# Kernel optimization log

Measured on AMD Instinct MI355X. Metric: run time of the kernel, lower is better.

Reference implementation:

```python
import jax, jax.numpy as jnp
import numpy as np

TEMP_LEN = 16
TARGET_LEN = 22
DIM = 768
HEADS = 12
B = 16
NT = TEMP_LEN * TEMP_LEN          # 256 template tokens
NG = TARGET_LEN * TARGET_LEN      # 484 target tokens
N = NT + NG                       # 740
POS_HID = 512


def _gaussian_heatmap(center, size, sig=1.0):
    x_axis = np.linspace(0, size[0] - 1, size[0]) - center[0]
    y_axis = np.linspace(0, size[1] - 1, size[1]) - center[1]
    xx, yy = np.meshgrid(x_axis, y_axis)
    return np.exp(-0.5 * (xx ** 2 + yy ** 2) / sig ** 2)


def _bias_index(L):
    # faithful to getBiasIndex (w_len == h_len here)
    coords = np.stack(np.meshgrid(np.arange(L), np.arange(L), indexing='ij'))  # [2,L,L]
    flat = coords.reshape(2, -1)                                               # [2,L*L]
    rel = (flat[:, :, None] - flat[:, None, :]).transpose(1, 2, 0).astype(np.int64)
    rel[:, :, 0] += L - 1
    rel[:, :, 1] += L - 1
    rel[:, :, 0] *= 2 * L - 1
    return rel.sum(-1)  # [L*L, L*L]


def setup_inputs() -> dict:
    key = jax.random.key(0)
    ks = jax.random.split(key, 12)
    f32 = jnp.float32
    x = jax.random.normal(ks[0], (B, N, DIM), dtype=f32)
    temp_q = jax.random.normal(ks[1], (B, NT, DIM), dtype=f32)
    target_q = jax.random.normal(ks[2], (B, NG, DIM), dtype=f32)
    # linear weights stored [in, out] (transposed torch layout)
    w = lambda k, i, o: jax.random.normal(k, (i, o), dtype=f32) * 0.02
    q_w = w(ks[3], DIM, DIM)
    k_w = w(ks[4], DIM, DIM)
    v_w = w(ks[5], DIM, DIM)
    proj_w = w(ks[6], DIM, DIM)
    proj_b = jnp.zeros((DIM,), dtype=f32)
    rpb_table = jax.random.normal(ks[7], ((2 * TARGET_LEN - 1) ** 2, HEADS), dtype=f32) * 0.0002
    rpb_table_temp = jax.random.normal(ks[8], ((2 * TEMP_LEN - 1) ** 2, HEADS), dtype=f32) * 0.0002
    pos_w1 = w(ks[9], 2, POS_HID)
    pos_b1 = jnp.zeros((POS_HID,), dtype=f32)
    pos_w2 = w(ks[10], POS_HID, HEADS)
    pos_b2 = jnp.zeros((HEADS,), dtype=f32)
    # deterministic cross-bias coordinate table (non-learned buffer)
    temp_tab = _gaussian_heatmap((TEMP_LEN // 2, TEMP_LEN // 2), (TEMP_LEN, TEMP_LEN)).astype(np.float32).flatten() \
        + np.linspace(-0.2, 0.2, NT, dtype=np.float32)
    targ_tab = _gaussian_heatmap((TARGET_LEN // 2, TARGET_LEN // 2), (TARGET_LEN, TARGET_LEN)).astype(np.float32).flatten() \
        + np.linspace(-0.2, 0.2, NG, dtype=np.float32)
    # torch.meshgrid default indexing='ij': [2, NT, NG] -> permute(1,2,0) -> [NT,NG,2]
    temp_target = np.stack(np.meshgrid(temp_tab, targ_tab, indexing='ij')).transpose(1, 2, 0)
    target_temp_tab = jnp.asarray(temp_target.transpose(1, 0, 2))  # [NG, NT, 2]
    temp_idx = jnp.asarray(_bias_index(TEMP_LEN))       # [NT, NT] int64
    target_idx = jnp.asarray(_bias_index(TARGET_LEN))   # [NG, NG] int64
    return {
        'x': x, 'temp_q': temp_q, 'target_q': target_q,
        'q_w': q_w, 'k_w': k_w, 'v_w': v_w, 'proj_w': proj_w, 'proj_b': proj_b,
        'rpb_table': rpb_table, 'rpb_table_temp': rpb_table_temp,
        'pos_w1': pos_w1, 'pos_b1': pos_b1, 'pos_w2': pos_w2, 'pos_b2': pos_b2,
        'target_temp_tab': target_temp_tab,
        'temp_idx': temp_idx, 'target_idx': target_idx,
    }


def reference(x, temp_q, target_q, q_w, k_w, v_w, proj_w, proj_b,
              rpb_table, rpb_table_temp, pos_w1, pos_b1, pos_w2, pos_b2,
              target_temp_tab, temp_idx, target_idx):
    Bsz, Ntok, C = x.shape
    H = HEADS
    hd = C // H
    scale = hd ** -0.5

    q_in = jnp.concatenate([temp_q, target_q], axis=1)                 # [B,N,C]
    q = (q_in @ q_w).reshape(Bsz, Ntok, H, hd).transpose(0, 2, 1, 3)   # [B,H,N,hd]
    k = (x @ k_w).reshape(Bsz, Ntok, H, hd).transpose(0, 2, 1, 3)
    v = (x @ v_w).reshape(Bsz, Ntok, H, hd).transpose(0, 2, 1, 3)

    # gathered relative position biases -> [H, Ni, Ni]
    temp_rpb = rpb_table_temp[temp_idx.reshape(-1)].reshape(NT, NT, H).transpose(2, 0, 1)
    targ_rpb = rpb_table[target_idx.reshape(-1)].reshape(NG, NG, H).transpose(2, 0, 1)
    # MLP cross bias: [NG, NT, 2] -> [NG, NT, H] -> [H, NG, NT]
    hid = jax.nn.relu(target_temp_tab @ pos_w1 + pos_b1)
    target_temp_bias = (hid @ pos_w2 + pos_b2).transpose(2, 0, 1)      # [H,NG,NT]
    temp_target_bias = target_temp_bias.transpose(0, 2, 1)             # [H,NT,NG]
    top = jnp.concatenate([temp_rpb, temp_target_bias], axis=2)        # [H,NT,N]
    bot = jnp.concatenate([target_temp_bias, targ_rpb], axis=2)        # [H,NG,N]
    bias = jnp.concatenate([top, bot], axis=1)[None]                   # [1,H,N,N]

    attn = jnp.einsum('bhnd,bhmd->bhnm', q, k) * scale + bias
    attn = jax.nn.softmax(attn, axis=-1)
    out = jnp.einsum('bhnm,bhmd->bhnd', attn, v).transpose(0, 2, 1, 3).reshape(Bsz, Ntok, C)
    return out @ proj_w + proj_b
```

## Files before the change

kernel.cpp:

```cpp
#include <hip/hip_runtime.h>


typedef unsigned short u16;
typedef short bf16x8 __attribute__((ext_vector_type(8)));
typedef float f32x4 __attribute__((ext_vector_type(4)));

#define BSZ   16
#define NTOK  740
#define NTMP  256
#define NTGT  484
#define DIMC  768
#define NHEAD 12
#define HDIM  64
#define MROWS (BSZ*NTOK)
#define SMAX  16.0f

__device__ __forceinline__ float bf2f(u16 u) {
    return __uint_as_float(((unsigned int)u) << 16);
}
__device__ __forceinline__ float bflo(unsigned int u) {
    return __uint_as_float(u << 16);
}
__device__ __forceinline__ float bfhi(unsigned int u) {
    return __uint_as_float(u & 0xffff0000u);
}
__device__ __forceinline__ u16 f2bf(float f) {
    unsigned int u = __float_as_uint(f);
    u += 0x7fffu + ((u >> 16) & 1u);
    return (u16)(u >> 16);
}

__device__ __forceinline__ void gl_lds16(const u16* g, u16* l) {
    __builtin_amdgcn_global_load_lds(
        (const __attribute__((address_space(1))) unsigned int*)(unsigned long long)g,
        (__attribute__((address_space(3))) unsigned int*)(unsigned int)(unsigned long long)l,
        16, 0, 0);
}

__device__ __forceinline__ size_t b2off(int h, int i, int j) {
    return ((size_t)(h * NTOK + i)) * 768 + ((j >> 6) << 6) + ((j & 15) << 2) + ((j >> 4) & 3);
}

#define PREP_CONV 4440
#define PREP_TRW  (PREP_CONV + 576)
#define PREP_DIAG (PREP_TRW + 2220)
#define PREP_ALL  (PREP_DIAG + 484)

__global__ __launch_bounds__(256) void prep_kernel(
    const float* __restrict__ x, const float* __restrict__ tq,
    const float* __restrict__ gq, u16* __restrict__ XB, u16* __restrict__ QB,
    const float* __restrict__ w0, const float* __restrict__ w1,
    const float* __restrict__ w2, const float* __restrict__ w3,
    u16* __restrict__ Wt,
    const float* __restrict__ rpb, const float* __restrict__ rpbt,
    const int* __restrict__ tidx, const int* __restrict__ gidx,
    const float* __restrict__ pw1, const float* __restrict__ pb1,
    const float* __restrict__ pw2, const float* __restrict__ pb2,
    const float* __restrict__ tab, u16* __restrict__ bias)
{
    __shared__ float T[64][65];
    const int blk = blockIdx.x;
    const int tid = threadIdx.x;

    if (blk < PREP_CONV) {
        int c = blk * 256 + tid;
        {
            const float* s = x + (size_t)c * 8;
            float4 p0 = *(const float4*)s, p1 = *(const float4*)(s + 4);
            u16 e[8] = {f2bf(p0.x), f2bf(p0.y), f2bf(p0.z), f2bf(p0.w),
                        f2bf(p1.x), f2bf(p1.y), f2bf(p1.z), f2bf(p1.w)};
            *(uint4*)(XB + (size_t)c * 8) = *(uint4*)e;
        }
        {
            int row = c / 96, cc = (c - row * 96) * 8;
            int b = row / NTOK, n = row - b * NTOK;
            const float* s = (n < NTMP)
                           ? tq + ((size_t)(b * NTMP + n)) * DIMC + cc
                           : gq + ((size_t)(b * NTGT + (n - NTMP))) * DIMC + cc;
            float4 p0 = *(const float4*)s, p1 = *(const float4*)(s + 4);
            u16 e[8] = {f2bf(p0.x), f2bf(p0.y), f2bf(p0.z), f2bf(p0.w),
                        f2bf(p1.x), f2bf(p1.y), f2bf(p1.z), f2bf(p1.w)};
            *(uint4*)(QB + (size_t)row * DIMC + cc) = *(uint4*)e;
        }
    } else if (blk < PREP_TRW) {
        int t = blk - PREP_CONV;
        int z = t / 144, rem = t - z * 144;
        int bx = rem % 12, by = rem / 12;
        const float* src = (z == 0) ? w0 : (z == 1) ? w1 : (z == 2) ? w2 : w3;
        const float scale = (z == 0) ? 0.125f : 1.0f;
        u16* dst = Wt + (size_t)z * DIMC * DIMC;
        int out0 = bx * 64, in0 = by * 64;
        #pragma unroll
        for (int l = 0; l < 4; l++) {
            int u = tid + (l << 8);
            int r = u >> 4, c4 = (u & 15) << 2;
            float4 p = *(const float4*)(src + (size_t)(in0 + r) * DIMC + out0 + c4);
            T[r][c4] = p.x; T[r][c4 + 1] = p.y; T[r][c4 + 2] = p.z; T[r][c4 + 3] = p.w;
        }
        __syncthreads();
        #pragma unroll
        for (int l = 0; l < 2; l++) {
            int u = tid + (l << 8);
            int r = u >> 3, c8 = (u & 7) << 3;
            u16 e[8];
            #pragma unroll
            for (int i = 0; i < 8; i++) e[i] = f2bf(T[c8 + i][r] * scale);
            *(uint4*)(dst + (size_t)(out0 + r) * DIMC + in0 + c8) = *(uint4*)e;
        }
    } else if (blk < PREP_DIAG) {
        int t = blk - PREP_TRW;
        int jb = t % 3, i = t / 3;
        int j = jb * 256 + tid;
        u16 vals[NHEAD];
        if (j >= NTOK) {
            u16 neg = f2bf(-1e30f);
            #pragma unroll
            for (int h = 0; h < NHEAD; h++) vals[h] = neg;
        } else if (i < NTMP && j < NTMP) {
            int idx = tidx[i * NTMP + j];
            #pragma unroll
            for (int h = 0; h < NHEAD; h++) vals[h] = f2bf(rpbt[idx * NHEAD + h]);
        } else if (i >= NTMP && j >= NTMP) {
            int idx = gidx[(i - NTMP) * NTGT + (j - NTMP)];
            #pragma unroll
            for (int h = 0; h < NHEAD; h++) vals[h] = f2bf(rpb[idx * NHEAD + h]);
        } else {
            return;
        }
        #pragma unroll
        for (int h = 0; h < NHEAD; h++) bias[b2off(h, i, j)] = vals[h];
    } else {
        int g = blk - PREP_DIAG;
        int t = tid;
        float a  = tab[(g * NTMP + t) * 2 + 0];
        float bb = tab[(g * NTMP + t) * 2 + 1];
        float acc[NHEAD];
        #pragma unroll
        for (int h = 0; h < NHEAD; h++) acc[h] = pb2[h];
        for (int k = 0; k < 512; k++) {
            float hid = fmaxf(a * pw1[k] + bb * pw1[512 + k] + pb1[k], 0.0f);
            #pragma unroll
            for (int h = 0; h < NHEAD; h++) acc[h] += hid * pw2[k * NHEAD + h];
        }
        #pragma unroll
        for (int h = 0; h < NHEAD; h++) {
            u16 v = f2bf(acc[h]);
            bias[b2off(h, t, NTMP + g)] = v;
            bias[b2off(h, NTMP + g, t)] = v;
        }
    }
}

template<int MODE>
__global__ __launch_bounds__(256) void gemm_bf16(
    const u16* __restrict__ A, const u16* __restrict__ Wt,
    const float* __restrict__ pb, u16* __restrict__ C0,
    u16* __restrict__ C1, float* __restrict__ Cf)
{
    __shared__ __align__(16) u16 As[8192];
    __shared__ __align__(16) u16 Bs[8192];
    const int tid = threadIdx.x;
    const int lane = tid & 63, w = tid >> 6;
    const int quad = lane >> 4, ln = lane & 15;
    const int m0 = blockIdx.y << 7;
    const int wm = (w >> 1) << 6, wn = (w & 1) << 6;

    const int nn = blockIdx.x << 7;
    const u16* Wbase = Wt + (size_t)nn * DIMC;
    u16* Cb;
    int col0;
    if (MODE == 1) {
        if (nn < DIMC) { col0 = nn; Cb = C0; }
        else           { col0 = nn - DIMC; Cb = C1; }
    } else {
        col0 = nn; Cb = C0;
    }

    f32x4 acc[4][4];
    #pragma unroll
    for (int i = 0; i < 4; i++)
        #pragma unroll
        for (int j = 0; j < 4; j++)
            acc[i][j] = (f32x4){0.f, 0.f, 0.f, 0.f};

    for (int k0 = 0; k0 < DIMC; k0 += 64) {
        __syncthreads();
        #pragma unroll
        for (int l = 0; l < 4; l++) {
            int f = tid + (l << 8);
            int c8 = f >> 7, r = f & 127;
            int grow = m0 + r; if (grow >= MROWS) grow = MROWS - 1;
            gl_lds16(A + (size_t)grow * DIMC + k0 + c8 * 8, As + f * 8);
            gl_lds16(Wbase + (size_t)r * DIMC + k0 + c8 * 8, Bs + f * 8);
        }
        __syncthreads();
        #pragma unroll
        for (int kp = 0; kp < 2; kp++) {
            bf16x8 af[4], bfr[4];
            #pragma unroll
            for (int mt = 0; mt < 4; mt++)
                af[mt] = *(const bf16x8*)&As[(((kp << 2) + quad) * 128 + wm + mt * 16 + ln) * 8];
            #pragma unroll
            for (int nt = 0; nt < 4; nt++)
                bfr[nt] = *(const bf16x8*)&Bs[(((kp << 2) + quad) * 128 + wn + nt * 16 + ln) * 8];
            #pragma unroll
            for (int mt = 0; mt < 4; mt++)
                #pragma unroll
                for (int nt = 0; nt < 4; nt++)
                    acc[mt][nt] = __builtin_amdgcn_mfma_f32_16x16x32_bf16(
                        af[mt], bfr[nt], acc[mt][nt], 0, 0, 0);
        }
    }

    #pragma unroll
    for (int mt = 0; mt < 4; mt++) {
        #pragma unroll
        for (int reg = 0; reg < 4; reg++) {
            int grow = m0 + wm + mt * 16 + (quad << 2) + reg;
            if (grow >= MROWS) continue;
            #pragma unroll
            for (int nt = 0; nt < 4; nt++) {
                int gcol = col0 + wn + nt * 16 + ln;
                float v = acc[mt][nt][reg];
                if (MODE == 2) {
                    Cf[(size_t)grow * DIMC + gcol] = v + pb[gcol];
                } else {
                    Cb[(size_t)grow * DIMC + gcol] = f2bf(v);
                }
            }
        }
    }
}

__global__ __launch_bounds__(256) void attn_mfma(
    const u16* __restrict__ Qg, const u16* __restrict__ Kg,
    const u16* __restrict__ Vg, const u16* __restrict__ bias,
    u16* __restrict__ ctx)
{
    __shared__ __align__(16) u16 KsL[4096];
    __shared__ __align__(16) u16 VtL[64 * 72];
    __shared__ __align__(16) u16 Pw[8][16][72];

    const int tid = threadIdx.x;
    const int lane = tid & 63, w = tid >> 6;
    const int quad = lane >> 4, ln = lane & 15;
    const int b = blockIdx.z, h = blockIdx.y;
    const int q0 = blockIdx.x << 7;
    const int mbase = q0 + (w << 5);
    const u16* bp = bias + ((size_t)h * NTOK) * 768;

    bf16x8 aq[2][2];
    #pragma unroll
    for (int mi = 0; mi < 2; mi++) {
        int qrow = mbase + (mi << 4) + ln; if (qrow >= NTOK) qrow = NTOK - 1;
        #pragma unroll
        for (int kp = 0; kp < 2; kp++)
            aq[mi][kp] = *(const bf16x8*)(Qg + ((size_t)(b * NTOK + qrow)) * DIMC
                                          + h * HDIM + kp * 32 + (quad << 3));
    }
    int boff[2][4];
    #pragma unroll
    for (int mi = 0; mi < 2; mi++)
        #pragma unroll
        for (int reg = 0; reg < 4; reg++) {
            int rr = mbase + (mi << 4) + (quad << 2) + reg;
            if (rr >= NTOK) rr = NTOK - 1;
            boff[mi][reg] = rr * 768 + (ln << 2);
        }

    const int pswz = ((ln >> 2) & 3) << 4;

    float rs[2][4] = {};
    f32x4 O[2][4];
    #pragma unroll
    for (int mi = 0; mi < 2; mi++)
        #pragma unroll
        for (int dt = 0; dt < 4; dt++) O[mi][dt] = (f32x4){0.f, 0.f, 0.f, 0.f};

    for (int j0 = 0; j0 < NTOK; j0 += 64) {
        __syncthreads();
        #pragma unroll
        for (int l = 0; l < 2; l++) {
            int f = tid + (l << 8);
            int chunk = f >> 6, jr = f & 63;
            int krow = j0 + jr; if (krow >= NTOK) krow = NTOK - 1;
            gl_lds16(Kg + ((size_t)(b * NTOK + krow)) * DIMC + h * HDIM + chunk * 8,
                     KsL + f * 8);
        }
        uint2 bvv[2][4];
        #pragma unroll
        for (int mi = 0; mi < 2; mi++)
            #pragma unroll
            for (int reg = 0; reg < 4; reg++)
                bvv[mi][reg] = *(const uint2*)(bp + boff[mi][reg] + j0);
        #pragma unroll
        for (int l = 0; l < 2; l++) {
            int u = tid + (l << 8);
            int jr = u >> 3, d0 = (u & 7) << 3;
            int vrow = j0 + jr; if (vrow >= NTOK) vrow = NTOK - 1;
            uint4 p = *(const uint4*)(Vg + ((size_t)(b * NTOK + vrow)) * DIMC + h * HDIM + d0);
            const u16* pe = (const u16*)&p;
            int jswz = jr ^ d0;
            #pragma unroll
            for (int i = 0; i < 8; i++) VtL[(d0 + i) * 72 + jswz] = pe[i];
        }
        __syncthreads();

        bf16x8 bv[4][2];
        #pragma unroll
        for (int dt = 0; dt < 4; dt++) {
            int key8 = ((dt * 2 + (ln >> 3)) & 7) << 3;
            #pragma unroll
            for (int kp = 0; kp < 2; kp++) {
                int koff = (kp * 32 + (quad << 3)) ^ key8;
                bv[dt][kp] = *(const bf16x8*)&VtL[(dt * 16 + ln) * 72 + koff];
            }
        }

        f32x4 s[2][4];
        #pragma unroll
        for (int mi = 0; mi < 2; mi++)
            #pragma unroll
            for (int nt = 0; nt < 4; nt++) s[mi][nt] = (f32x4){0.f, 0.f, 0.f, 0.f};
        #pragma unroll
        for (int kp = 0; kp < 2; kp++)
            #pragma unroll
            for (int nt = 0; nt < 4; nt++) {
                bf16x8 bk = *(const bf16x8*)
                    &KsL[(((kp << 2) + quad) * 64 + nt * 16 + ln) * 8];
                s[0][nt] = __builtin_amdgcn_mfma_f32_16x16x32_bf16(aq[0][kp], bk, s[0][nt], 0, 0, 0);
                s[1][nt] = __builtin_amdgcn_mfma_f32_16x16x32_bf16(aq[1][kp], bk, s[1][nt], 0, 0, 0);
            }

        #pragma unroll
        for (int mi = 0; mi < 2; mi++) {
            #pragma unroll
            for (int reg = 0; reg < 4; reg++) {
                uint2 bb = bvv[mi][reg];
                float p0 = __expf(s[mi][0][reg] + bflo(bb.x) - SMAX);
                float p1 = __expf(s[mi][1][reg] + bfhi(bb.x) - SMAX);
                float p2 = __expf(s[mi][2][reg] + bflo(bb.y) - SMAX);
                float p3 = __expf(s[mi][3][reg] + bfhi(bb.y) - SMAX);
                s[mi][0][reg] = p0; s[mi][1][reg] = p1;
                s[mi][2][reg] = p2; s[mi][3][reg] = p3;
                rs[mi][reg] += p0 + p1 + p2 + p3;
            }
            u16* pwb = &Pw[(w << 1) + mi][0][0];
            #pragma unroll
            for (int nt = 0; nt < 4; nt++) {
                int colw = ((nt ^ quad) << 4) + ln;
                #pragma unroll
                for (int reg = 0; reg < 4; reg++)
                    pwb[((quad << 2) + reg) * 72 + colw] = f2bf(s[mi][nt][reg]);
            }
            bf16x8 ap[2];
            #pragma unroll
            for (int kp = 0; kp < 2; kp++) {
                int koff = (kp * 32 + (quad << 3)) ^ pswz;
                ap[kp] = *(const bf16x8*)&pwb[ln * 72 + koff];
            }
            #pragma unroll
            for (int dt = 0; dt < 4; dt++)
                #pragma unroll
                for (int kp = 0; kp < 2; kp++)
                    O[mi][dt] = __builtin_amdgcn_mfma_f32_16x16x32_bf16(
                        ap[kp], bv[dt][kp], O[mi][dt], 0, 0, 0);
        }
    }

    #pragma unroll
    for (int mi = 0; mi < 2; mi++) {
        #pragma unroll
        for (int reg = 0; reg < 4; reg++) {
            float t = rs[mi][reg];
            #pragma unroll
            for (int mk = 8; mk >= 1; mk >>= 1) t += __shfl_xor(t, mk);
            float inv = 1.0f / t;
            int row = mbase + (mi << 4) + (quad << 2) + reg;
            if (row < NTOK) {
                #pragma unroll
                for (int dt = 0; dt < 4; dt++)
                    ctx[((size_t)(b * NTOK + row)) * DIMC + h * HDIM + dt * 16 + ln]
                        = f2bf(O[mi][dt][reg] * inv);
            }
        }
    }
}

extern "C" void kernel_launch(void* const* d_in, const int* in_sizes, int n_in,
                              void* d_out, int out_size, void* d_ws, size_t ws_size,
                              hipStream_t stream)
{
    const float* x        = (const float*)d_in[0];
    const float* temp_q   = (const float*)d_in[1];
    const float* target_q = (const float*)d_in[2];
    const float* q_w      = (const float*)d_in[3];
    const float* k_w      = (const float*)d_in[4];
    const float* v_w      = (const float*)d_in[5];
    const float* proj_w   = (const float*)d_in[6];
    const float* proj_b   = (const float*)d_in[7];
    const float* rpb      = (const float*)d_in[8];
    const float* rpbt     = (const float*)d_in[9];
    const float* pw1      = (const float*)d_in[10];
    const float* pb1      = (const float*)d_in[11];
    const float* pw2      = (const float*)d_in[12];
    const float* pb2      = (const float*)d_in[13];
    const float* tab      = (const float*)d_in[14];
    const int*   tidx     = (const int*)d_in[15];
    const int*   gidx     = (const int*)d_in[16];
    float* out = (float*)d_out;

    char* ws = (char*)d_ws;
    const size_t S = (size_t)MROWS * DIMC * sizeof(u16);
    const size_t SZB = (size_t)NHEAD * NTOK * 768 * sizeof(u16);
    u16* XB    = (u16*)(ws);
    u16* QB    = (u16*)(ws + S);
    u16* Q     = (u16*)(ws + 2 * S);
    u16* K     = (u16*)(ws + 3 * S);
    u16* V     = QB;
    u16* CTX   = XB;
    u16* BIAS2 = (u16*)(ws + 4 * S);
    u16* WT    = (u16*)(ws + 4 * S + SZB);

    prep_kernel<<<dim3(PREP_ALL), 256, 0, stream>>>(
        x, temp_q, target_q, XB, QB,
        q_w, k_w, v_w, proj_w, WT,
        rpb, rpbt, tidx, gidx,
        pw1, pb1, pw2, pb2, tab, BIAS2);

    const u16* WTq = WT;
    const u16* WTk = WT + (size_t)DIMC * DIMC;
    const u16* WTp = WT + 3 * (size_t)DIMC * DIMC;

    gemm_bf16<0><<<dim3(6, 93), 256, 0, stream>>>(QB, WTq, nullptr, Q, nullptr, nullptr);
    gemm_bf16<1><<<dim3(12, 93), 256, 0, stream>>>(XB, WTk, nullptr, K, V, nullptr);
    attn_mfma<<<dim3(6, 12, 16), 256, 0, stream>>>(Q, K, V, BIAS2, CTX);
    gemm_bf16<2><<<dim3(6, 93), 256, 0, stream>>>(CTX, WTp, proj_b, nullptr, nullptr, out);
}
```

Before: 496.4 us.

## Double-buffer GEMM LDS tiles and remap workgroups across XCDs

The GEMM main loop now uses two LDS buffers so the next K-tile's global-to-LDS loads are issued while the current tile is being multiplied. This hides load latency and removes one barrier per iteration. Workgroup IDs are also remapped so that consecutive tiles land on the same XCD, which should improve L2 reuse of the shared A/W tiles. The cost is doubled LDS use (64KB per block), which may lower occupancy. Whether the async loads truly overlap depends on how waitcnt is handled around the barriers.

Result: faster. 469.4 us (-5.4%).

```diff
diff --git a/kernel.cpp b/kernel.cpp
--- a/kernel.cpp
+++ b/kernel.cpp
@@ -157,15 +157,25 @@
     const float* __restrict__ pb, u16* __restrict__ C0,
     u16* __restrict__ C1, float* __restrict__ Cf)
 {
-    __shared__ __align__(16) u16 As[8192];
-    __shared__ __align__(16) u16 Bs[8192];
+    __shared__ __align__(16) u16 As[2][8192];
+    __shared__ __align__(16) u16 Bs[2][8192];
     const int tid = threadIdx.x;
     const int lane = tid & 63, w = tid >> 6;
     const int quad = lane >> 4, ln = lane & 15;
-    const int m0 = blockIdx.y << 7;
+
+    const int gx = gridDim.x;
+    const int nwg = gx * (int)gridDim.y;
+    const int flat = blockIdx.y * gx + blockIdx.x;
+    const int q = nwg >> 3, r = nwg & 7;
+    const int xcd = flat & 7, sidx = flat >> 3;
+    const int wg = (xcd < r) ? xcd * (q + 1) + sidx
+                             : r * (q + 1) + (xcd - r) * q + sidx;
+    const int by = wg / gx, bx = wg - by * gx;
+
+    const int m0 = by << 7;
     const int wm = (w >> 1) << 6, wn = (w & 1) << 6;
 
-    const int nn = blockIdx.x << 7;
+    const int nn = bx << 7;
     const u16* Wbase = Wt + (size_t)nn * DIMC;
     u16* Cb;
     int col0;
@@ -183,34 +193,50 @@
         for (int j = 0; j < 4; j++)
             acc[i][j] = (f32x4){0.f, 0.f, 0.f, 0.f};
 
-    for (int k0 = 0; k0 < DIMC; k0 += 64) {
+#define STAGE(s, k0) do {                                                     \
+    _Pragma("unroll")                                                         \
+    for (int l = 0; l < 4; l++) {                                             \
+        int f = tid + (l << 8);                                  \
+        int c8 = f >> 7, rr = f & 127;                                        \
+        int grow = m0 + rr; if (grow >= MROWS) grow = MROWS - 1;              \
+        gl_lds16(A + (size_t)grow * DIMC + (k0) + c8 * 8, &As[s][f * 8]);     \
+        gl_lds16(Wbase + (size_t)rr * DIMC + (k0) + c8 * 8, &Bs[s][f * 8]);   \
+    } } while (0)
+
+#define COMPUTE(s) do {                                                       \
+    _Pragma("unroll")                                                         \
+    for (int kp = 0; kp < 2; kp++) {                                          \
+        bf16x8 af[4], bfr[4];                                                 \
+        _Pragma("unroll")                                                     \
+        for (int mt = 0; mt < 4; mt++)                                        \
+            af[mt] = *(const bf16x8*)                                         \
+                &As[s][(((kp << 2) + quad) * 128 + wm + mt * 16 + ln) * 8];   \
+        _Pragma("unroll")                                                     \
+        for (int nt = 0; nt < 4; nt++)                                        \
+            bfr[nt] = *(const bf16x8*)                                        \
+                &Bs[s][(((kp << 2) + quad) * 128 + wn + nt * 16 + ln) * 8];   \
+        _Pragma("unroll")                                                     \
+        for (int mt = 0; mt < 4; mt++)                                        \
+            _Pragma("unroll")                                                 \
+            for (int nt = 0; nt < 4; nt++)                                    \
+                acc[mt][nt] = __builtin_amdgcn_mfma_f32_16x16x32_bf16(        \
+                    af[mt], bfr[nt], acc[mt][nt], 0, 0, 0);                   \
+    } } while (0)
+
+    STAGE(0, 0);
+    __syncthreads();
+    #pragma unroll 1
+    for (int t = 0; t < 12; t += 2) {
+        STAGE(1, (t + 1) << 6);
+        COMPUTE(0);
         __syncthreads();
-        #pragma unroll
-        for (int l = 0; l < 4; l++) {
-            int f = tid + (l << 8);
-            int c8 = f >> 7, r = f & 127;
-            int grow = m0 + r; if (grow >= MROWS) grow = MROWS - 1;
-            gl_lds16(A + (size_t)grow * DIMC + k0 + c8 * 8, As + f * 8);
-            gl_lds16(Wbase + (size_t)r * DIMC + k0 + c8 * 8, Bs + f * 8);
-        }
+        if (t < 10) STAGE(0, (t + 2) << 6);
+        COMPUTE(1);
         __syncthreads();
-        #pragma unroll
-        for (int kp = 0; kp < 2; kp++) {
-            bf16x8 af[4], bfr[4];
-            #pragma unroll
-            for (int mt = 0; mt < 4; mt++)
-                af[mt] = *(const bf16x8*)&As[(((kp << 2) + quad) * 128 + wm + mt * 16 + ln) * 8];
-            #pragma unroll
-            for (int nt = 0; nt < 4; nt++)
-                bfr[nt] = *(const bf16x8*)&Bs[(((kp << 2) + quad) * 128 + wn + nt * 16 + ln) * 8];
-            #pragma unroll
-            for (int mt = 0; mt < 4; mt++)
-                #pragma unroll
-                for (int nt = 0; nt < 4; nt++)
-                    acc[mt][nt] = __builtin_amdgcn_mfma_f32_16x16x32_bf16(
-                        af[mt], bfr[nt], acc[mt][nt], 0, 0, 0);
-        }
-    }
+    }
+
+#undef STAGE
+#undef COMPUTE
 
     #pragma unroll
     for (int mt = 0; mt < 4; mt++) {
```
